# Optimization experiments

Hardware: AMD Instinct MI355X
Metric: run time of the kernel (lower is better)

The kernel has to match this reference:

```python
import jax, jax.numpy as jnp
import numpy as np

B, N, M, DIN, H = 8, 2048, 2048, 512, 256
SCALE = float(np.sqrt(H))


def _lin_params(key, din, dout):
    kw, kb = jax.random.split(key)
    lim = 1.0 / np.sqrt(din)
    W = jax.random.uniform(kw, (din, dout), jnp.float32, -lim, lim)
    b = jax.random.uniform(kb, (dout,), jnp.float32, -lim, lim)
    return W, b


def setup_inputs() -> dict:
    key = jax.random.key(0)
    ks = jax.random.split(key, 16)
    inp = {
        "q_fp": jax.random.normal(ks[0], (B, N, DIN), jnp.float32),
        "v_ret": jax.random.normal(ks[1], (B, M, DIN), jnp.float32),
        "pi_star": jax.random.uniform(ks[2], (B, N, M), jnp.float32),
    }
    names = ["qs", "ks", "vs", "qe", "ke", "ve"]
    for i, nm in enumerate(names):
        W, b = _lin_params(ks[3 + i], DIN, H)
        inp[f"W{nm}"], inp[f"b{nm}"] = W, b
    inp["W1"], inp["b1"] = _lin_params(ks[10], 4 * H, H)
    inp["W2"], inp["b2"] = _lin_params(ks[11], H, H)
    inp["gamma"] = jnp.ones((1,), jnp.float32)
    inp["ew"] = jnp.array(1.0, jnp.float32)
    return inp


def _forward(q_fp, v_ret, pi_star, Wqs, bqs, Wks, bks, Wvs, bvs,
             Wqe, bqe, Wke, bke, Wve, bve, W1, b1, W2, b2, gamma, ew):
    q_struct = q_fp @ Wqs + bqs          # [B,N,H]
    k_struct = v_ret @ Wks + bks         # [B,M,H]
    v_struct = v_ret @ Wvs + bvs
    q_elec = q_fp @ Wqe + bqe
    k_elec = v_ret @ Wke + bke
    v_elec = v_ret @ Wve + bve

    structural_logits = jnp.einsum("bnh,bmh->bnm", q_struct, k_struct) / SCALE

    # cdist(p=2) via the quadratic expansion, clamped for numeric safety
    q2 = jnp.sum(q_elec * q_elec, -1, keepdims=True)          # [B,N,1]
    k2 = jnp.sum(k_elec * k_elec, -1, keepdims=True)          # [B,M,1]
    d2 = q2 + jnp.swapaxes(k2, -2, -1) - 2.0 * jnp.einsum("bnh,bmh->bnm", q_elec, k_elec)
    electronic_distance = jnp.sqrt(jnp.maximum(d2, 1e-12))    # [B,N,M]
    electronic_scale = jnp.maximum(
        electronic_distance.mean(axis=(-2, -1), keepdims=True), 1e-4)
    electronic_logits = -(electronic_distance / electronic_scale)

    pi_mask = gamma * jnp.log(jnp.maximum(pi_star, 1e-9))
    final_logits = structural_logits + ew * electronic_logits + pi_mask
    attn = jax.nn.softmax(final_logits, axis=-1)              # [B,N,M]

    ctx_s = jnp.einsum("bnm,bmh->bnh", attn, v_struct)
    ctx_e = jnp.einsum("bnm,bmh->bnh", attn, v_elec)
    fused = jnp.concatenate([ctx_s, ctx_e, ctx_s - ctx_e, ctx_s * ctx_e], axis=-1)
    h = jax.nn.silu(fused @ W1 + b1)
    return h @ W2 + b2


def reference(q_fp, v_ret, pi_star, Wqs, bqs, Wks, bks, Wvs, bvs,
              Wqe, bqe, Wke, bke, Wve, bve, W1, b1, W2, b2, gamma, ew):
    return _forward(q_fp, v_ret, pi_star, Wqs, bqs, Wks, bks, Wvs, bvs,
                    Wqe, bqe, Wke, bke, Wve, bve, W1, b1, W2, b2, gamma, ew)
```

## Files before the change

### kernel.cpp

```cpp
#include <hip/hip_runtime.h>

#define Bsz 8
#define Nq  2048
#define Mk  2048
#define BKt 32

typedef __attribute__((ext_vector_type(8))) short   short8;
typedef __attribute__((ext_vector_type(4))) float   floatx4;

__device__ __forceinline__ unsigned short f2bf(float f) {
  union { float f; unsigned u; } x; x.f = f;
  unsigned r = x.u + 0x7fffu + ((x.u >> 16) & 1u);
  return (unsigned short)(r >> 16);
}
__device__ __forceinline__ float bf2f(unsigned short s) {
  union { unsigned u; float f; } x; x.u = ((unsigned)s) << 16;
  return x.f;
}

__device__ __forceinline__ void gload16(const unsigned short* g, unsigned short* l) {
  __builtin_amdgcn_global_load_lds(
      (const __attribute__((address_space(1))) void*)g,
      (__attribute__((address_space(3))) void*)l, 16, 0, 0);
}

__device__ __forceinline__ void gemm_core_nt(
    const unsigned short* __restrict__ A, int lda,
    const unsigned short* __restrict__ B, int ldb,
    int K, unsigned short* ldsA, unsigned short* ldsB,
    floatx4 (&acc)[4][4])
{
  const int tid  = threadIdx.x;
  const int lane = tid & 63;
  const int wid  = tid >> 6;
  const int wm   = wid & 1;
  const int wn   = wid >> 1;
  const int fr   = lane & 15;
  const int fk   = (lane >> 4) << 3;
  const int lr   = lane >> 2;
  const int lc   = (lane & 3) << 3;
  const int r0   = wid << 5;

  const unsigned short* gA0 = A + (size_t)(r0 + lr) * lda + lc;
  const unsigned short* gA1 = gA0 + (size_t)16 * lda;
  const unsigned short* gB0 = B + (size_t)(r0 + lr) * ldb + lc;
  const unsigned short* gB1 = gB0 + (size_t)16 * ldb;
  unsigned short* lA0 = ldsA + (r0     ) * BKt;
  unsigned short* lA1 = ldsA + (r0 + 16) * BKt;
  unsigned short* lB0 = ldsB + (r0     ) * BKt;
  unsigned short* lB1 = ldsB + (r0 + 16) * BKt;
  const unsigned short* fa = ldsA + (wm * 64 + fr) * BKt + fk;
  const unsigned short* fb = ldsB + (wn * 64 + fr) * BKt + fk;

  for (int k0 = 0; k0 < K; k0 += BKt) {
    __syncthreads();
    gload16(gA0, lA0); gA0 += BKt;
    gload16(gA1, lA1); gA1 += BKt;
    gload16(gB0, lB0); gB0 += BKt;
    gload16(gB1, lB1); gB1 += BKt;
    __syncthreads();
    short8 af[4], bfr[4];
#pragma unroll
    for (int i = 0; i < 4; i++) af[i]  = *(const short8*)(fa + i * 16 * BKt);
#pragma unroll
    for (int i = 0; i < 4; i++) bfr[i] = *(const short8*)(fb + i * 16 * BKt);
#pragma unroll
    for (int i = 0; i < 4; i++)
#pragma unroll
      for (int j = 0; j < 4; j++)
        acc[i][j] = __builtin_amdgcn_mfma_f32_16x16x32_bf16(af[i], bfr[j], acc[i][j], 0, 0, 0);
  }
}

#define EPILOGUE_VARS \
  const int lane = threadIdx.x & 63; \
  const int wid  = threadIdx.x >> 6; \
  const int wm   = wid & 1; \
  const int wn   = wid >> 1; \
  const int r4   = (lane >> 4) * 4;  \
  const int cn   = lane & 15; \
  (void)wid;

__global__ __launch_bounds__(256, 2) void k_proj(
    const float* __restrict__ A, const unsigned short* __restrict__ Bw,
    const float* __restrict__ bias, unsigned short* __restrict__ Cout,
    int Ncols, int K)
{
  __shared__ alignas(16) unsigned short ldsA[128 * BKt];
  __shared__ alignas(16) unsigned short ldsB[128 * BKt];
  floatx4 acc[4][4];
#pragma unroll
  for (int i = 0; i < 4; i++)
#pragma unroll
    for (int j = 0; j < 4; j++)
#pragma unroll
      for (int t = 0; t < 4; t++) acc[i][j][t] = 0.f;

  const int tid = threadIdx.x;
  const int ar  = tid >> 1;
  const int ac  = (tid & 1) << 4;

  const int lane = tid & 63;
  const int wid  = tid >> 6;
  const int wm   = wid & 1;
  const int wn   = wid >> 1;
  const int fr   = lane & 15;
  const int fk   = (lane >> 4) << 3;
  const int lr   = lane >> 2;
  const int lc   = (lane & 3) << 3;
  const int r0   = wid << 5;

  const float* ap = A + ((size_t)blockIdx.x * 128 + ar) * K + ac;
  const unsigned short* gB0 = Bw + ((size_t)blockIdx.y * 128 + r0 + lr) * K + lc;
  const unsigned short* gB1 = gB0 + (size_t)16 * K;
  unsigned short* lB0 = ldsB + (r0     ) * BKt;
  unsigned short* lB1 = ldsB + (r0 + 16) * BKt;
  uint4* sa = (uint4*)(ldsA + ar * BKt + ac);
  const unsigned short* fa = ldsA + (wm * 64 + fr) * BKt + fk;
  const unsigned short* fb = ldsB + (wn * 64 + fr) * BKt + fk;

  for (int k0 = 0; k0 < K; k0 += BKt) {
    float4 f0 = *(const float4*)(ap + 0);
    float4 f1 = *(const float4*)(ap + 4);
    float4 f2 = *(const float4*)(ap + 8);
    float4 f3 = *(const float4*)(ap + 12);
    ap += BKt;
    uint4 pa, pb;
    pa.x = f2bf(f0.x) | ((unsigned)f2bf(f0.y) << 16);
    pa.y = f2bf(f0.z) | ((unsigned)f2bf(f0.w) << 16);
    pa.z = f2bf(f1.x) | ((unsigned)f2bf(f1.y) << 16);
    pa.w = f2bf(f1.z) | ((unsigned)f2bf(f1.w) << 16);
    pb.x = f2bf(f2.x) | ((unsigned)f2bf(f2.y) << 16);
    pb.y = f2bf(f2.z) | ((unsigned)f2bf(f2.w) << 16);
    pb.z = f2bf(f3.x) | ((unsigned)f2bf(f3.y) << 16);
    pb.w = f2bf(f3.z) | ((unsigned)f2bf(f3.w) << 16);
    __syncthreads();
    gload16(gB0, lB0); gB0 += BKt;
    gload16(gB1, lB1); gB1 += BKt;
    sa[0] = pa; sa[1] = pb;
    __syncthreads();
    short8 af[4], bfr[4];
#pragma unroll
    for (int i = 0; i < 4; i++) af[i]  = *(const short8*)(fa + i * 16 * BKt);
#pragma unroll
    for (int i = 0; i < 4; i++) bfr[i] = *(const short8*)(fb + i * 16 * BKt);
#pragma unroll
    for (int i = 0; i < 4; i++)
#pragma unroll
      for (int j = 0; j < 4; j++)
        acc[i][j] = __builtin_amdgcn_mfma_f32_16x16x32_bf16(af[i], bfr[j], acc[i][j], 0, 0, 0);
  }

  const int r4 = (lane >> 4) * 4;
  const int cn = lane & 15;
#pragma unroll
  for (int i = 0; i < 4; i++) {
#pragma unroll
    for (int j = 0; j < 4; j++) {
      int gc = blockIdx.y * 128 + wn * 64 + j * 16 + cn;
      float bv = bias[gc];
#pragma unroll
      for (int r = 0; r < 4; r++) {
        int gr = blockIdx.x * 128 + wm * 64 + i * 16 + r4 + r;
        Cout[(size_t)gr * Ncols + gc] = f2bf(acc[i][j][r] + bv);
      }
    }
  }
}

template<int MODE>
__global__ __launch_bounds__(256, 3) void k_gemm_bias(
    const unsigned short* __restrict__ A, const unsigned short* __restrict__ Bw,
    const float* __restrict__ bias, void* __restrict__ Cout, int Ncols, int K)
{
  __shared__ alignas(16) unsigned short ldsA[128 * BKt];
  __shared__ alignas(16) unsigned short ldsB[128 * BKt];
  floatx4 acc[4][4];
#pragma unroll
  for (int i = 0; i < 4; i++)
#pragma unroll
    for (int j = 0; j < 4; j++)
#pragma unroll
      for (int t = 0; t < 4; t++) acc[i][j][t] = 0.f;

  const unsigned short* Ab = A + (size_t)blockIdx.x * 128 * K;
  const unsigned short* Bb = Bw + (size_t)blockIdx.y * 128 * K;
  gemm_core_nt(Ab, K, Bb, K, K, ldsA, ldsB, acc);

  EPILOGUE_VARS
#pragma unroll
  for (int i = 0; i < 4; i++) {
#pragma unroll
    for (int j = 0; j < 4; j++) {
      int gc = blockIdx.y * 128 + wn * 64 + j * 16 + cn;
      float bv = bias[gc];
#pragma unroll
      for (int r = 0; r < 4; r++) {
        int gr = blockIdx.x * 128 + wm * 64 + i * 16 + r4 + r;
        float v = acc[i][j][r] + bv;
        if constexpr (MODE == 1) v = v / (1.f + __expf(-v));
        if constexpr (MODE == 2)
          ((float*)Cout)[(size_t)gr * Ncols + gc] = v;
        else
          ((unsigned short*)Cout)[(size_t)gr * Ncols + gc] = f2bf(v);
      }
    }
  }
}

__global__ __launch_bounds__(256, 2) void k_sd(
    const unsigned short* __restrict__ Xq, const unsigned short* __restrict__ Xk,
    const float* __restrict__ q2, const float* __restrict__ k2,
    int b0, float* __restrict__ dsum, unsigned* __restrict__ sd)
{
  __shared__ alignas(16) unsigned short ldsA[128 * BKt];
  __shared__ alignas(16) unsigned short ldsB[128 * BKt];
  floatx4 accS[4][4], accE[4][4];
#pragma unroll
  for (int i = 0; i < 4; i++)
#pragma unroll
    for (int j = 0; j < 4; j++)
#pragma unroll
      for (int t = 0; t < 4; t++) { accS[i][j][t] = 0.f; accE[i][j][t] = 0.f; }

  const int z = blockIdx.z;
  const int b = b0 + z;
  const unsigned short* Aq = Xq + ((size_t)(b * Nq) + blockIdx.x * 128) * 512;
  const unsigned short* Bk = Xk + ((size_t)(b * Mk) + blockIdx.y * 128) * 1024;
  gemm_core_nt(Aq,       512, Bk,       1024, 256, ldsA, ldsB, accS);
  gemm_core_nt(Aq + 256, 512, Bk + 512, 1024, 256, ldsA, ldsB, accE);

  EPILOGUE_VARS
  float kkv[4];
#pragma unroll
  for (int j = 0; j < 4; j++)
    kkv[j] = k2[b * Mk + blockIdx.y * 128 + wn * 64 + j * 16 + cn];

  float lsum = 0.f;
#pragma unroll
  for (int i = 0; i < 4; i++) {
#pragma unroll
    for (int r = 0; r < 4; r++) {
      const int n = blockIdx.x * 128 + wm * 64 + i * 16 + r4 + r;
      const float qq = q2[b * Nq + n];
      unsigned* srow = sd + (size_t)(z * Nq + n) * Mk;
#pragma unroll
      for (int j = 0; j < 4; j++) {
        const int m = blockIdx.y * 128 + wn * 64 + j * 16 + cn;
        float d = sqrtf(fmaxf(qq + kkv[j] - 2.f * accE[i][j][r], 1e-12f));
        lsum += d;
        srow[m] = (unsigned)f2bf(accS[i][j][r] * 0.0625f)
                | ((unsigned)f2bf(d) << 16);
      }
    }
  }
#pragma unroll
  for (int o = 32; o; o >>= 1) lsum += __shfl_down(lsum, o);
  __syncthreads();
  float* red = (float*)ldsA;
  if (lane == 0) red[wid] = lsum;
  __syncthreads();
  if (threadIdx.x == 0) atomicAdd(dsum + b, red[0] + red[1] + red[2] + red[3]);
}

__global__ __launch_bounds__(256) void k_softmax(
    const unsigned* __restrict__ sd, const float* __restrict__ pi,
    const float* __restrict__ dsum, const float* __restrict__ gamma_p,
    const float* __restrict__ ew_p, int b0,
    unsigned short* __restrict__ attn, float* __restrict__ rowsum)
{
  const int wid  = threadIdx.x >> 6;
  const int lane = threadIdx.x & 63;
  const int rl   = blockIdx.x * 4 + wid;
  const int b    = b0 + (rl >> 11);
  const int n    = rl & 2047;

  const float scale = fmaxf(dsum[b] * (1.f / (2048.f * 2048.f)), 1e-4f);
  const float einv  = ew_p[0] / scale;
  const float gv    = gamma_p[0];
  const bool  g1    = (gv == 1.0f);

  const unsigned*  sp = sd  + (size_t)rl * Mk;
  const float*     pp = pi  + ((size_t)b * Nq + n) * Mk;
  unsigned short*  ap = attn + ((size_t)b * Nq + n) * Mk;

  float rs = 0.f;
  for (int it = 0; it < 8; ++it) {
    const int c = it * 256 + lane * 4;
    const uint4  sv = *(const uint4*)(sp + c);
    const float4 pv = *(const float4*)(pp + c);
    const unsigned uu[4]  = {sv.x, sv.y, sv.z, sv.w};
    const float    pp4[4] = {pv.x, pv.y, pv.z, pv.w};
    float e[4];
#pragma unroll
    for (int t = 0; t < 4; ++t) {
      union { unsigned u; float f; } cs, cd;
      cs.u = uu[t] << 16;
      cd.u = uu[t] & 0xffff0000u;
      float p  = fmaxf(pp4[t], 1e-9f);
      float pf = g1 ? p : __expf(gv * __logf(p));
      e[t] = __expf(cs.f - einv * cd.f) * pf;
      rs += e[t];
    }
    uint2 st;
    st.x = (unsigned)f2bf(e[0]) | ((unsigned)f2bf(e[1]) << 16);
    st.y = (unsigned)f2bf(e[2]) | ((unsigned)f2bf(e[3]) << 16);
    *(uint2*)(ap + c) = st;
  }
#pragma unroll
  for (int o = 32; o; o >>= 1) rs += __shfl_down(rs, o);
  if (lane == 0) rowsum[b * Nq + n] = rs;
}

__global__ __launch_bounds__(256, 3) void k_pv(
    const unsigned short* __restrict__ At, const unsigned short* __restrict__ VT,
    const float* __restrict__ rowsum, unsigned short* __restrict__ ctx)
{
  __shared__ alignas(16) unsigned short ldsA[128 * BKt];
  __shared__ alignas(16) unsigned short ldsB[128 * BKt];
  floatx4 acc[4][4];
#pragma unroll
  for (int i = 0; i < 4; i++)
#pragma unroll
    for (int j = 0; j < 4; j++)
#pragma unroll
      for (int t = 0; t < 4; t++) acc[i][j][t] = 0.f;

  const int b = blockIdx.z;
  const unsigned short* Ab = At + ((size_t)b * Nq + blockIdx.x * 128) * (size_t)Mk;
  const unsigned short* Bb = VT + ((size_t)b * 512 + blockIdx.y * 128) * (size_t)Mk;
  gemm_core_nt(Ab, Mk, Bb, Mk, Mk, ldsA, ldsB, acc);

  EPILOGUE_VARS
  const int rowbase = b * Nq + blockIdx.x * 128 + wm * 64;
#pragma unroll
  for (int i = 0; i < 4; i++) {
    float rinv[4];
#pragma unroll
    for (int r = 0; r < 4; r++)
      rinv[r] = 1.f / rowsum[rowbase + i * 16 + r4 + r];
#pragma unroll
    for (int j = 0; j < 4; j++) {
      int gc = blockIdx.y * 128 + wn * 64 + j * 16 + cn;
#pragma unroll
      for (int r = 0; r < 4; r++) {
        int gr = blockIdx.x * 128 + wm * 64 + i * 16 + r4 + r;
        ctx[((size_t)b * Nq + gr) * 512 + gc] = f2bf(acc[i][j][r] * rinv[r]);
      }
    }
  }
}

__global__ void k_prep_w(
    const float* __restrict__ Wqs, const float* __restrict__ Wqe,
    const float* __restrict__ Wks, const float* __restrict__ Wvs,
    const float* __restrict__ Wke, const float* __restrict__ Wve,
    const float* __restrict__ W1,  const float* __restrict__ W2,
    const float* __restrict__ bqs, const float* __restrict__ bqe,
    const float* __restrict__ bks, const float* __restrict__ bvs,
    const float* __restrict__ bke, const float* __restrict__ bve,
    unsigned short* __restrict__ WqT, unsigned short* __restrict__ WkT,
    unsigned short* __restrict__ W1T, unsigned short* __restrict__ W2T,
    float* __restrict__ bq, float* __restrict__ bk, float* __restrict__ dsum)
{
  int gid = blockIdx.x * 256 + threadIdx.x;
  int idx = gid;
  if (idx < 512 * 512) {
    int j = idx >> 9, k = idx & 511;
    float v = (j < 256) ? Wqs[k * 256 + j] : Wqe[k * 256 + (j - 256)];
    WqT[idx] = f2bf(v);
  } else if ((idx -= 512 * 512) < 1024 * 512) {
    int j = idx >> 9, k = idx & 511;
    int s = j >> 8, jj = j & 255;
    const float* Wp = (s == 0) ? Wks : (s == 1) ? Wvs : (s == 2) ? Wke : Wve;
    WkT[idx] = f2bf(Wp[k * 256 + jj]);
  } else if ((idx -= 1024 * 512) < 256 * 1024) {
    int j = idx >> 10, k = idx & 1023;
    W1T[idx] = f2bf(W1[k * 256 + j]);
  } else if ((idx -= 256 * 1024) < 256 * 256) {
    int j = idx >> 8, k = idx & 255;
    W2T[idx] = f2bf(W2[k * 256 + j]);
  }
  if (gid < 512)  bq[gid] = (gid < 256) ? bqs[gid] : bqe[gid - 256];
  if (gid < 1024) bk[gid] = (gid < 256) ? bks[gid]
                    : (gid < 512) ? bvs[gid - 256]
                    : (gid < 768) ? bke[gid - 512] : bve[gid - 768];
  if (gid < 8) dsum[gid] = 0.f;
}

__global__ __launch_bounds__(256) void k_rowsq(
    const unsigned short* __restrict__ X, int stride, int colOff, float* __restrict__ out)
{
  int row = blockIdx.x * 4 + (threadIdx.x >> 6);
  int lane = threadIdx.x & 63;
  const unsigned short* p = X + (size_t)row * stride + colOff + lane * 4;
  uint2 u = *(const uint2*)p;
  float a0 = bf2f((unsigned short)(u.x & 0xffff));
  float a1 = bf2f((unsigned short)(u.x >> 16));
  float a2 = bf2f((unsigned short)(u.y & 0xffff));
  float a3 = bf2f((unsigned short)(u.y >> 16));
  float s = a0 * a0 + a1 * a1 + a2 * a2 + a3 * a3;
#pragma unroll
  for (int o = 32; o; o >>= 1) s += __shfl_down(s, o);
  if (lane == 0) out[row] = s;
}

__global__ void k_trans_vt(const unsigned short* __restrict__ Xk, unsigned short* __restrict__ VT) {
  __shared__ unsigned short t[32][33];
  const int b = blockIdx.z;
  const int m0 = blockIdx.x * 32, j0 = blockIdx.y * 32;
  const int tx = threadIdx.x, ty = threadIdx.y;
#pragma unroll
  for (int i = 0; i < 4; i++) {
    int m = m0 + ty + i * 8;
    int j = j0 + tx;
    int c = (j < 256) ? (256 + j) : (512 + j);
    t[ty + i * 8][tx] = Xk[((size_t)b * Mk + m) * 1024 + c];
  }
  __syncthreads();
#pragma unroll
  for (int i = 0; i < 4; i++) {
    int j = j0 + ty + i * 8;
    int m = m0 + tx;
    VT[((size_t)b * 512 + j) * Mk + m] = t[tx][ty + i * 8];
  }
}

__global__ void k_fused(const unsigned short* __restrict__ ctx, unsigned short* __restrict__ fused) {
  int idx = blockIdx.x * 256 + threadIdx.x;
  int bn = idx >> 8;
  int j = idx & 255;
  float cs = bf2f(ctx[(size_t)bn * 512 + j]);
  float ce = bf2f(ctx[(size_t)bn * 512 + 256 + j]);
  size_t o = (size_t)bn * 1024 + j;
  fused[o]       = f2bf(cs);
  fused[o + 256] = f2bf(ce);
  fused[o + 512] = f2bf(cs - ce);
  fused[o + 768] = f2bf(cs * ce);
}

extern "C" void kernel_launch(void* const* d_in, const int* in_sizes, int n_in,
                              void* d_out, int out_size, void* d_ws, size_t ws_size,
                              hipStream_t stream) {
  (void)in_sizes; (void)n_in; (void)out_size; (void)ws_size;
  const float* q_fp  = (const float*)d_in[0];
  const float* v_ret = (const float*)d_in[1];
  const float* pi    = (const float*)d_in[2];
  const float* Wqs = (const float*)d_in[3];  const float* bqs = (const float*)d_in[4];
  const float* Wks = (const float*)d_in[5];  const float* bks = (const float*)d_in[6];
  const float* Wvs = (const float*)d_in[7];  const float* bvs = (const float*)d_in[8];
  const float* Wqe = (const float*)d_in[9];  const float* bqe = (const float*)d_in[10];
  const float* Wke = (const float*)d_in[11]; const float* bke = (const float*)d_in[12];
  const float* Wve = (const float*)d_in[13]; const float* bve = (const float*)d_in[14];
  const float* W1  = (const float*)d_in[15]; const float* b1  = (const float*)d_in[16];
  const float* W2  = (const float*)d_in[17]; const float* b2  = (const float*)d_in[18];
  const float* gamma = (const float*)d_in[19];
  const float* ew    = (const float*)d_in[20];

  char* w = (char*)d_ws;
  unsigned short* WqT = (unsigned short*)(w + 0);
  unsigned short* WkT = (unsigned short*)(w + 524288);
  unsigned short* W1T = (unsigned short*)(w + 1572864);
  unsigned short* W2T = (unsigned short*)(w + 2097152);
  float* bq   = (float*)(w + 2228224);
  float* bk   = (float*)(w + 2230272);
  float* q2   = (float*)(w + 2234368);
  float* k2   = (float*)(w + 2299904);
  float* dsum = (float*)(w + 2365440);
  unsigned short* ctx  = (unsigned short*)(w + 2365696);
  unsigned short* hbuf = (unsigned short*)(w + 19142912);
  unsigned short* Xq = (unsigned short*)(w + 35920128);
  unsigned short* Xk = (unsigned short*)(w + 52697344);
  unsigned short* VT = (unsigned short*)(w + 86251776);
  unsigned short* attn = (unsigned short*)(w + 103028992);
  unsigned short* fused = attn;
  unsigned* sdbuf = (unsigned*)(w + 2365696);
  float* rowsum = (float*)d_out;

  k_prep_w<<<4352, 256, 0, stream>>>(Wqs, Wqe, Wks, Wvs, Wke, Wve, W1, W2,
                                     bqs, bqe, bks, bvs, bke, bve,
                                     WqT, WkT, W1T, W2T, bq, bk, dsum);
  k_proj<<<dim3(128, 4), 256, 0, stream>>>(q_fp,  WqT, bq, Xq, 512, 512);
  k_proj<<<dim3(128, 8), 256, 0, stream>>>(v_ret, WkT, bk, Xk, 1024, 512);
  k_rowsq<<<4096, 256, 0, stream>>>(Xq, 512, 256, q2);
  k_rowsq<<<4096, 256, 0, stream>>>(Xk, 1024, 512, k2);
  for (int c = 0; c < 4; ++c) {
    k_sd<<<dim3(16, 16, 2), 256, 0, stream>>>(Xq, Xk, q2, k2, 2 * c, dsum, sdbuf);
    k_softmax<<<1024, 256, 0, stream>>>(sdbuf, pi, dsum, gamma, ew, 2 * c,
                                        attn, rowsum);
  }
  k_trans_vt<<<dim3(64, 16, 8), dim3(32, 8), 0, stream>>>(Xk, VT);
  k_pv<<<dim3(16, 4, 8), 256, 0, stream>>>(attn, VT, rowsum, ctx);
  k_fused<<<16384, 256, 0, stream>>>(ctx, fused);
  k_gemm_bias<1><<<dim3(128, 2), 256, 0, stream>>>(fused, W1T, b1, hbuf, 256, 1024);
  k_gemm_bias<2><<<dim3(128, 2), 256, 0, stream>>>(hbuf, W2T, b2, d_out, 256, 256);
}
```

Baseline: 572.8 us.

## Use 8-wave 512-thread blocks for all MFMA GEMMs and swizzle PV tiles

Each 128x128 tile is now computed by 8 waves instead of 4, so every wave owns a 64x32 sub-tile, loads half as much per step, and holds half the accumulators. This applies to the projection, score/distance, PV and MLP GEMMs, and the launch bounds are raised to allow more resident waves. The aim is higher occupancy and better latency hiding in the single-buffered, sync-heavy K loop. The PV kernel also reorders its blocks through a swizzled 1-D index so that concurrently running blocks share attention rows in cache. In exchange, each wave does fewer MFMAs per LDS fragment load, and more waves contend at each barrier.

```diff
diff --git a/kernel.cpp b/kernel.cpp
--- a/kernel.cpp
+++ b/kernel.cpp
@@ -24,11 +24,11 @@
       (__attribute__((address_space(3))) void*)l, 16, 0, 0);
 }
 
-__device__ __forceinline__ void gemm_core_nt(
+__device__ __forceinline__ void gemm_core8_nt(
     const unsigned short* __restrict__ A, int lda,
     const unsigned short* __restrict__ B, int ldb,
     int K, unsigned short* ldsA, unsigned short* ldsB,
-    floatx4 (&acc)[4][4])
+    floatx4 (&acc)[4][2])
 {
   const int tid  = threadIdx.x;
   const int lane = tid & 63;
@@ -39,35 +39,29 @@
   const int fk   = (lane >> 4) << 3;
   const int lr   = lane >> 2;
   const int lc   = (lane & 3) << 3;
-  const int r0   = wid << 5;
-
-  const unsigned short* gA0 = A + (size_t)(r0 + lr) * lda + lc;
-  const unsigned short* gA1 = gA0 + (size_t)16 * lda;
-  const unsigned short* gB0 = B + (size_t)(r0 + lr) * ldb + lc;
-  const unsigned short* gB1 = gB0 + (size_t)16 * ldb;
-  unsigned short* lA0 = ldsA + (r0     ) * BKt;
-  unsigned short* lA1 = ldsA + (r0 + 16) * BKt;
-  unsigned short* lB0 = ldsB + (r0     ) * BKt;
-  unsigned short* lB1 = ldsB + (r0 + 16) * BKt;
+  const int r0   = wid << 4;
+
+  const unsigned short* gA = A + (size_t)(r0 + lr) * lda + lc;
+  const unsigned short* gB = B + (size_t)(r0 + lr) * ldb + lc;
+  unsigned short* lA = ldsA + r0 * BKt;
+  unsigned short* lB = ldsB + r0 * BKt;
   const unsigned short* fa = ldsA + (wm * 64 + fr) * BKt + fk;
-  const unsigned short* fb = ldsB + (wn * 64 + fr) * BKt + fk;
+  const unsigned short* fb = ldsB + (wn * 32 + fr) * BKt + fk;
 
   for (int k0 = 0; k0 < K; k0 += BKt) {
     __syncthreads();
-    gload16(gA0, lA0); gA0 += BKt;
-    gload16(gA1, lA1); gA1 += BKt;
-    gload16(gB0, lB0); gB0 += BKt;
-    gload16(gB1, lB1); gB1 += BKt;
+    gload16(gA, lA); gA += BKt;
+    gload16(gB, lB); gB += BKt;
     __syncthreads();
-    short8 af[4], bfr[4];
+    short8 af[4], bfr[2];
 #pragma unroll
     for (int i = 0; i < 4; i++) af[i]  = *(const short8*)(fa + i * 16 * BKt);
 #pragma unroll
-    for (int i = 0; i < 4; i++) bfr[i] = *(const short8*)(fb + i * 16 * BKt);
+    for (int j = 0; j < 2; j++) bfr[j] = *(const short8*)(fb + j * 16 * BKt);
 #pragma unroll
     for (int i = 0; i < 4; i++)
 #pragma unroll
-      for (int j = 0; j < 4; j++)
+      for (int j = 0; j < 2; j++)
         acc[i][j] = __builtin_amdgcn_mfma_f32_16x16x32_bf16(af[i], bfr[j], acc[i][j], 0, 0, 0);
   }
 }
@@ -81,25 +75,22 @@
   const int cn   = lane & 15; \
   (void)wid;
 
-__global__ __launch_bounds__(256, 2) void k_proj(
+__global__ __launch_bounds__(512, 4) void k_proj(
     const float* __restrict__ A, const unsigned short* __restrict__ Bw,
     const float* __restrict__ bias, unsigned short* __restrict__ Cout,
     int Ncols, int K)
 {
   __shared__ alignas(16) unsigned short ldsA[128 * BKt];
   __shared__ alignas(16) unsigned short ldsB[128 * BKt];
-  floatx4 acc[4][4];
+  floatx4 acc[4][2];
 #pragma unroll
   for (int i = 0; i < 4; i++)
 #pragma unroll
-    for (int j = 0; j < 4; j++)
+    for (int j = 0; j < 2; j++)
 #pragma unroll
       for (int t = 0; t < 4; t++) acc[i][j][t] = 0.f;
 
-  const int tid = threadIdx.x;
-  const int ar  = tid >> 1;
-  const int ac  = (tid & 1) << 4;
-
+  const int tid  = threadIdx.x;
   const int lane = tid & 63;
   const int wid  = tid >> 6;
   const int wm   = wid & 1;
@@ -108,46 +99,37 @@
   const int fk   = (lane >> 4) << 3;
   const int lr   = lane >> 2;
   const int lc   = (lane & 3) << 3;
-  const int r0   = wid << 5;
-
-  const float* ap = A + ((size_t)blockIdx.x * 128 + ar) * K + ac;
-  const unsigned short* gB0 = Bw + ((size_t)blockIdx.y * 128 + r0 + lr) * K + lc;
-  const unsigned short* gB1 = gB0 + (size_t)16 * K;
-  unsigned short* lB0 = ldsB + (r0     ) * BKt;
-  unsigned short* lB1 = ldsB + (r0 + 16) * BKt;
-  uint4* sa = (uint4*)(ldsA + ar * BKt + ac);
+  const int r0   = wid << 4;
+
+  const float* ap = A + ((size_t)blockIdx.x * 128 + r0 + lr) * K + lc;
+  const unsigned short* gB = Bw + ((size_t)blockIdx.y * 128 + r0 + lr) * K + lc;
+  unsigned short* lB = ldsB + r0 * BKt;
+  uint4* sa = (uint4*)(ldsA + (r0 + lr) * BKt + lc);
   const unsigned short* fa = ldsA + (wm * 64 + fr) * BKt + fk;
-  const unsigned short* fb = ldsB + (wn * 64 + fr) * BKt + fk;
+  const unsigned short* fb = ldsB + (wn * 32 + fr) * BKt + fk;
 
   for (int k0 = 0; k0 < K; k0 += BKt) {
     float4 f0 = *(const float4*)(ap + 0);
     float4 f1 = *(const float4*)(ap + 4);
-    float4 f2 = *(const float4*)(ap + 8);
-    float4 f3 = *(const float4*)(ap + 12);
     ap += BKt;
-    uint4 pa, pb;
+    uint4 pa;
     pa.x = f2bf(f0.x) | ((unsigned)f2bf(f0.y) << 16);
     pa.y = f2bf(f0.z) | ((unsigned)f2bf(f0.w) << 16);
     pa.z = f2bf(f1.x) | ((unsigned)f2bf(f1.y) << 16);
     pa.w = f2bf(f1.z) | ((unsigned)f2bf(f1.w) << 16);
-    pb.x = f2bf(f2.x) | ((unsigned)f2bf(f2.y) << 16);
-    pb.y = f2bf(f2.z) | ((unsigned)f2bf(f2.w) << 16);
-    pb.z = f2bf(f3.x) | ((unsigned)f2bf(f3.y) << 16);
-    pb.w = f2bf(f3.z) | ((unsigned)f2bf(f3.w) << 16);
     __syncthreads();
-    gload16(gB0, lB0); gB0 += BKt;
-    gload16(gB1, lB1); gB1 += BKt;
-    sa[0] = pa; sa[1] = pb;
+    gload16(gB, lB); gB += BKt;
+    *sa = pa;
     __syncthreads();
-    short8 af[4], bfr[4];
+    short8 af[4], bfr[2];
 #pragma unroll
     for (int i = 0; i < 4; i++) af[i]  = *(const short8*)(fa + i * 16 * BKt);
 #pragma unroll
-    for (int i = 0; i < 4; i++) bfr[i] = *(const short8*)(fb + i * 16 * BKt);
+    for (int j = 0; j < 2; j++) bfr[j] = *(const short8*)(fb + j * 16 * BKt);
 #pragma unroll
     for (int i = 0; i < 4; i++)
 #pragma unroll
-      for (int j = 0; j < 4; j++)
+      for (int j = 0; j < 2; j++)
         acc[i][j] = __builtin_amdgcn_mfma_f32_16x16x32_bf16(af[i], bfr[j], acc[i][j], 0, 0, 0);
   }
 
@@ -156,8 +138,8 @@
 #pragma unroll
   for (int i = 0; i < 4; i++) {
 #pragma unroll
-    for (int j = 0; j < 4; j++) {
-      int gc = blockIdx.y * 128 + wn * 64 + j * 16 + cn;
+    for (int j = 0; j < 2; j++) {
+      int gc = blockIdx.y * 128 + wn * 32 + j * 16 + cn;
       float bv = bias[gc];
 #pragma unroll
       for (int r = 0; r < 4; r++) {
@@ -169,30 +151,30 @@
 }
 
 template<int MODE>
-__global__ __launch_bounds__(256, 3) void k_gemm_bias(
+__global__ __launch_bounds__(512, 4) void k_gemm_bias(
     const unsigned short* __restrict__ A, const unsigned short* __restrict__ Bw,
     const float* __restrict__ bias, void* __restrict__ Cout, int Ncols, int K)
 {
   __shared__ alignas(16) unsigned short ldsA[128 * BKt];
   __shared__ alignas(16) unsigned short ldsB[128 * BKt];
-  floatx4 acc[4][4];
+  floatx4 acc[4][2];
 #pragma unroll
   for (int i = 0; i < 4; i++)
 #pragma unroll
-    for (int j = 0; j < 4; j++)
+    for (int j = 0; j < 2; j++)
 #pragma unroll
       for (int t = 0; t < 4; t++) acc[i][j][t] = 0.f;
 
   const unsigned short* Ab = A + (size_t)blockIdx.x * 128 * K;
   const unsigned short* Bb = Bw + (size_t)blockIdx.y * 128 * K;
-  gemm_core_nt(Ab, K, Bb, K, K, ldsA, ldsB, acc);
+  gemm_core8_nt(Ab, K, Bb, K, K, ldsA, ldsB, acc);
 
   EPILOGUE_VARS
 #pragma unroll
   for (int i = 0; i < 4; i++) {
 #pragma unroll
-    for (int j = 0; j < 4; j++) {
-      int gc = blockIdx.y * 128 + wn * 64 + j * 16 + cn;
+    for (int j = 0; j < 2; j++) {
+      int gc = blockIdx.y * 128 + wn * 32 + j * 16 + cn;
       float bv = bias[gc];
 #pragma unroll
       for (int r = 0; r < 4; r++) {
@@ -208,18 +190,18 @@
   }
 }
 
-__global__ __launch_bounds__(256, 2) void k_sd(
+__global__ __launch_bounds__(512, 4) void k_sd(
     const unsigned short* __restrict__ Xq, const unsigned short* __restrict__ Xk,
     const float* __restrict__ q2, const float* __restrict__ k2,
     int b0, float* __restrict__ dsum, unsigned* __restrict__ sd)
 {
   __shared__ alignas(16) unsigned short ldsA[128 * BKt];
   __shared__ alignas(16) unsigned short ldsB[128 * BKt];
-  floatx4 accS[4][4], accE[4][4];
+  floatx4 accS[4][2], accE[4][2];
 #pragma unroll
   for (int i = 0; i < 4; i++)
 #pragma unroll
-    for (int j = 0; j < 4; j++)
+    for (int j = 0; j < 2; j++)
 #pragma unroll
       for (int t = 0; t < 4; t++) { accS[i][j][t] = 0.f; accE[i][j][t] = 0.f; }
 
@@ -227,14 +209,13 @@
   const int b = b0 + z;
   const unsigned short* Aq = Xq + ((size_t)(b * Nq) + blockIdx.x * 128) * 512;
   const unsigned short* Bk = Xk + ((size_t)(b * Mk) + blockIdx.y * 128) * 1024;
-  gemm_core_nt(Aq,       512, Bk,       1024, 256, ldsA, ldsB, accS);
-  gemm_core_nt(Aq + 256, 512, Bk + 512, 1024, 256, ldsA, ldsB, accE);
+  gemm_core8_nt(Aq,       512, Bk,       1024, 256, ldsA, ldsB, accS);
+  gemm_core8_nt(Aq + 256, 512, Bk + 512, 1024, 256, ldsA, ldsB, accE);
 
   EPILOGUE_VARS
-  float kkv[4];
-#pragma unroll
-  for (int j = 0; j < 4; j++)
-    kkv[j] = k2[b * Mk + blockIdx.y * 128 + wn * 64 + j * 16 + cn];
+  const int colT = blockIdx.y * 128 + wn * 32;
+  const float kk0 = k2[b * Mk + colT + cn];
+  const float kk1 = k2[b * Mk + colT + 16 + cn];
 
   float lsum = 0.f;
 #pragma unroll
@@ -245,9 +226,9 @@
       const float qq = q2[b * Nq + n];
       unsigned* srow = sd + (size_t)(z * Nq + n) * Mk;
 #pragma unroll
-      for (int j = 0; j < 4; j++) {
-        const int m = blockIdx.y * 128 + wn * 64 + j * 16 + cn;
-        float d = sqrtf(fmaxf(qq + kkv[j] - 2.f * accE[i][j][r], 1e-12f));
+      for (int j = 0; j < 2; j++) {
+        const int m = colT + j * 16 + cn;
+        float d = sqrtf(fmaxf(qq + (j ? kk1 : kk0) - 2.f * accE[i][j][r], 1e-12f));
         lsum += d;
         srow[m] = (unsigned)f2bf(accS[i][j][r] * 0.0625f)
                 | ((unsigned)f2bf(d) << 16);
@@ -260,7 +241,12 @@
   float* red = (float*)ldsA;
   if (lane == 0) red[wid] = lsum;
   __syncthreads();
-  if (threadIdx.x == 0) atomicAdd(dsum + b, red[0] + red[1] + red[2] + red[3]);
+  if (threadIdx.x == 0) {
+    float s = 0.f;
+#pragma unroll
+    for (int t = 0; t < 8; t++) s += red[t];
+    atomicAdd(dsum + b, s);
+  }
 }
 
 __global__ __launch_bounds__(256) void k_softmax(
@@ -312,27 +298,31 @@
   if (lane == 0) rowsum[b * Nq + n] = rs;
 }
 
-__global__ __launch_bounds__(256, 3) void k_pv(
+__global__ __launch_bounds__(512, 4) void k_pv(
     const unsigned short* __restrict__ At, const unsigned short* __restrict__ VT,
     const float* __restrict__ rowsum, unsigned short* __restrict__ ctx)
 {
   __shared__ alignas(16) unsigned short ldsA[128 * BKt];
   __shared__ alignas(16) unsigned short ldsB[128 * BKt];
-  floatx4 acc[4][4];
+  floatx4 acc[4][2];
 #pragma unroll
   for (int i = 0; i < 4; i++)
 #pragma unroll
-    for (int j = 0; j < 4; j++)
+    for (int j = 0; j < 2; j++)
 #pragma unroll
       for (int t = 0; t < 4; t++) acc[i][j][t] = 0.f;
 
-  const int b = blockIdx.z;
-  const unsigned short* Ab = At + ((size_t)b * Nq + blockIdx.x * 128) * (size_t)Mk;
-  const unsigned short* Bb = VT + ((size_t)b * 512 + blockIdx.y * 128) * (size_t)Mk;
-  gemm_core_nt(Ab, Mk, Bb, Mk, Mk, ldsA, ldsB, acc);
+  const int l  = blockIdx.x;
+  const int lg = ((l & 7) << 3) | (l >> 3);
+  const int tx = lg >> 2;
+  const int ty = lg & 3;
+  const int b  = blockIdx.z;
+  const unsigned short* Ab = At + ((size_t)b * Nq + tx * 128) * (size_t)Mk;
+  const unsigned short* Bb = VT + ((size_t)b * 512 + ty * 128) * (size_t)Mk;
+  gemm_core8_nt(Ab, Mk, Bb, Mk, Mk, ldsA, ldsB, acc);
 
   EPILOGUE_VARS
-  const int rowbase = b * Nq + blockIdx.x * 128 + wm * 64;
+  const int rowbase = b * Nq + tx * 128 + wm * 64;
 #pragma unroll
   for (int i = 0; i < 4; i++) {
     float rinv[4];
@@ -340,11 +330,11 @@
     for (int r = 0; r < 4; r++)
       rinv[r] = 1.f / rowsum[rowbase + i * 16 + r4 + r];
 #pragma unroll
-    for (int j = 0; j < 4; j++) {
-      int gc = blockIdx.y * 128 + wn * 64 + j * 16 + cn;
+    for (int j = 0; j < 2; j++) {
+      int gc = ty * 128 + wn * 32 + j * 16 + cn;
 #pragma unroll
       for (int r = 0; r < 4; r++) {
-        int gr = blockIdx.x * 128 + wm * 64 + i * 16 + r4 + r;
+        int gr = tx * 128 + wm * 64 + i * 16 + r4 + r;
         ctx[((size_t)b * Nq + gr) * 512 + gc] = f2bf(acc[i][j][r] * rinv[r]);
       }
     }
@@ -480,18 +470,18 @@
   k_prep_w<<<4352, 256, 0, stream>>>(Wqs, Wqe, Wks, Wvs, Wke, Wve, W1, W2,
                                      bqs, bqe, bks, bvs, bke, bve,
                                      WqT, WkT, W1T, W2T, bq, bk, dsum);
-  k_proj<<<dim3(128, 4), 256, 0, stream>>>(q_fp,  WqT, bq, Xq, 512, 512);
-  k_proj<<<dim3(128, 8), 256, 0, stream>>>(v_ret, WkT, bk, Xk, 1024, 512);
+  k_proj<<<dim3(128, 4), 512, 0, stream>>>(q_fp,  WqT, bq, Xq, 512, 512);
+  k_proj<<<dim3(128, 8), 512, 0, stream>>>(v_ret, WkT, bk, Xk, 1024, 512);
   k_rowsq<<<4096, 256, 0, stream>>>(Xq, 512, 256, q2);
   k_rowsq<<<4096, 256, 0, stream>>>(Xk, 1024, 512, k2);
   for (int c = 0; c < 4; ++c) {
-    k_sd<<<dim3(16, 16, 2), 256, 0, stream>>>(Xq, Xk, q2, k2, 2 * c, dsum, sdbuf);
+    k_sd<<<dim3(16, 16, 2), 512, 0, stream>>>(Xq, Xk, q2, k2, 2 * c, dsum, sdbuf);
     k_softmax<<<1024, 256, 0, stream>>>(sdbuf, pi, dsum, gamma, ew, 2 * c,
                                         attn, rowsum);
   }
   k_trans_vt<<<dim3(64, 16, 8), dim3(32, 8), 0, stream>>>(Xk, VT);
-  k_pv<<<dim3(16, 4, 8), 256, 0, stream>>>(attn, VT, rowsum, ctx);
+  k_pv<<<dim3(64, 1, 8), 512, 0, stream>>>(attn, VT, rowsum, ctx);
   k_fused<<<16384, 256, 0, stream>>>(ctx, fused);
-  k_gemm_bias<1><<<dim3(128, 2), 256, 0, stream>>>(fused, W1T, b1, hbuf, 256, 1024);
-  k_gemm_bias<2><<<dim3(128, 2), 256, 0, stream>>>(hbuf, W2T, b2, d_out, 256, 256);
-}
+  k_gemm_bias<1><<<dim3(128, 2), 512, 0, stream>>>(fused, W1T, b1, hbuf, 256, 1024);
+  k_gemm_bias<2><<<dim3(128, 2), 512, 0, stream>>>(hbuf, W2T, b2, d_out, 256, 256);
+}
```

Result: no change. 567.5 us (-0.9%).
